# Kernel optimization log

Measured on AMD Instinct MI355X. Metric: run time of the kernel, lower is better.

## Reference

```python
import jax, jax.numpy as jnp
import numpy as np

N_NODES = 50000
N_EDGES = 800000
D_IN, H, D_OUT = 128, 128, 64


def setup_inputs() -> dict:
    key = jax.random.key(0)
    ks = jax.random.split(key, 8)
    x = jax.random.normal(ks[0], (N_NODES, D_IN), dtype=jnp.float32)
    edge_index = jax.random.randint(ks[1], (2, N_EDGES), 0, N_NODES, dtype=jnp.int64)
    s = 0.05
    return {
        "x": x,
        "edge_index": edge_index,
        # PyG Linear weights are [out, in]; y = x @ W.T + b
        "W_rel1": jax.random.normal(ks[2], (H, D_IN), dtype=jnp.float32) * s,
        "W_root1": jax.random.normal(ks[3], (H, D_IN), dtype=jnp.float32) * s,
        "b1": jax.random.normal(ks[4], (H,), dtype=jnp.float32) * s,
        "W_rel2": jax.random.normal(ks[5], (D_OUT, H), dtype=jnp.float32) * s,
        "W_root2": jax.random.normal(ks[6], (D_OUT, H), dtype=jnp.float32) * s,
        "b2": jax.random.normal(ks[7], (D_OUT,), dtype=jnp.float32) * s,
    }


def graph_conv(x, src, dst, W_rel, W_root, b):
    # sum-aggregate raw neighbor features, then apply linear (equivalent to
    # transforming each message first, but cheaper: one gather + one GEMM).
    agg = jax.ops.segment_sum(x[src], dst, num_segments=N_NODES)  # [N, D]
    return jnp.einsum('nd,hd->nh', agg, W_rel) \
         + jnp.einsum('nd,hd->nh', x, W_root) + b


def reference(x, edge_index, W_rel1, W_root1, b1, W_rel2, W_root2, b2):
    src, dst = edge_index[0], edge_index[1]  # messages flow src -> dst
    t = jax.nn.relu(graph_conv(x, src, dst, W_rel1, W_root1, b1))
    t = graph_conv(t, src, dst, W_rel2, W_root2, b2)
    return t
```

## Files before the change

### kernel.cpp

```cpp
#include <hip/hip_runtime.h>

#define NNODES 50000
#define DIM 128
#define SCAN_CHUNK 4096
#define NSCAN 13
#define PREP_BLOCKS 3200
#define POISON ((int)0xAAAAAAAA)

typedef __attribute__((ext_vector_type(8))) __bf16 bf16x8;
typedef __attribute__((ext_vector_type(4))) float f32x4;

__device__ inline unsigned short f2b(float f) {
    unsigned int u = __float_as_uint(f);
    u += 0x7fffu + ((u >> 16) & 1u);
    return (unsigned short)(u >> 16);
}
__device__ inline float blo(unsigned int u) { return __uint_as_float(u << 16); }
__device__ inline float bhi(unsigned int u) { return __uint_as_float(u & 0xffff0000u); }
__device__ inline unsigned int pack2(float a, float b) {
    return (unsigned int)f2b(a) | ((unsigned int)f2b(b) << 16);
}

__global__ __launch_bounds__(256) void k_prep(
    const float* __restrict__ x, unsigned short* __restrict__ xb, int n4,
    const float* __restrict__ Wa1, const float* __restrict__ Wb1,
    const float* __restrict__ Wa2, const float* __restrict__ Wb2,
    unsigned short* __restrict__ wa1, unsigned short* __restrict__ wb1,
    unsigned short* __restrict__ wa2, unsigned short* __restrict__ wb2,
    const int* __restrict__ dst, int* __restrict__ counts,
    unsigned short* __restrict__ rank, int n_edges)
{
    const int gid = blockIdx.x * 256 + threadIdx.x;

    const int i1 = blockIdx.x * 512 + threadIdx.x;
    const int i2 = i1 + 256;
    const bool ok1 = i1 < n4, ok2 = i2 < n4;
    float4 v1, v2;
    if (ok1) v1 = reinterpret_cast<const float4*>(x)[i1];
    if (ok2) v2 = reinterpret_cast<const float4*>(x)[i2];

    if (gid < n_edges) {
        const int rep = threadIdx.x & 3;
        int rk = atomicAdd(&counts[rep * NNODES + dst[gid]], 1) - POISON;
        rank[gid] = (unsigned short)(rk | (rep << 14));
    }

    if (gid < 16384) { wa1[gid] = f2b(Wa1[gid]); wb1[gid] = f2b(Wb1[gid]); }
    if (gid < 8192)  { wa2[gid] = f2b(Wa2[gid]); wb2[gid] = f2b(Wb2[gid]); }

    if (ok1) {
        uint2 o;
        o.x = pack2(v1.x, v1.y);
        o.y = pack2(v1.z, v1.w);
        reinterpret_cast<uint2*>(xb)[i1] = o;
    }
    if (ok2) {
        uint2 o;
        o.x = pack2(v2.x, v2.y);
        o.y = pack2(v2.z, v2.w);
        reinterpret_cast<uint2*>(xb)[i2] = o;
    }
}

__global__ __launch_bounds__(1024) void k_scan_local(
    const int* __restrict__ counts, int* __restrict__ rowptr,
    int* __restrict__ bsum, uint2* __restrict__ repx2, int n)
{
    __shared__ int wsum[16];
    const int lane = threadIdx.x & 63;
    const int wid = threadIdx.x >> 6;
    int i = blockIdx.x * SCAN_CHUNK + threadIdx.x * 4;
    int4 v = make_int4(0, 0, 0, 0);
    if (i + 3 < n) {
        int4 c0 = *reinterpret_cast<const int4*>(counts + i);
        int4 c1 = *reinterpret_cast<const int4*>(counts + NNODES + i);
        int4 c2 = *reinterpret_cast<const int4*>(counts + 2 * NNODES + i);
        int4 c3 = *reinterpret_cast<const int4*>(counts + 3 * NNODES + i);
        c0.x -= POISON; c0.y -= POISON; c0.z -= POISON; c0.w -= POISON;
        c1.x -= POISON; c1.y -= POISON; c1.z -= POISON; c1.w -= POISON;
        c2.x -= POISON; c2.y -= POISON; c2.z -= POISON; c2.w -= POISON;
        c3.x -= POISON; c3.y -= POISON; c3.z -= POISON; c3.w -= POISON;
        v.x = c0.x + c1.x + c2.x + c3.x;
        v.y = c0.y + c1.y + c2.y + c3.y;
        v.z = c0.z + c1.z + c2.z + c3.z;
        v.w = c0.w + c1.w + c2.w + c3.w;
        uint2 r0, r1g, r2g, r3g;
        r0.x  = (unsigned)(c0.x) << 16;
        r0.y  = (unsigned)(c0.x + c1.x) | ((unsigned)(c0.x + c1.x + c2.x) << 16);
        r1g.x = (unsigned)(c0.y) << 16;
        r1g.y = (unsigned)(c0.y + c1.y) | ((unsigned)(c0.y + c1.y + c2.y) << 16);
        r2g.x = (unsigned)(c0.z) << 16;
        r2g.y = (unsigned)(c0.z + c1.z) | ((unsigned)(c0.z + c1.z + c2.z) << 16);
        r3g.x = (unsigned)(c0.w) << 16;
        r3g.y = (unsigned)(c0.w + c1.w) | ((unsigned)(c0.w + c1.w + c2.w) << 16);
        repx2[i + 0] = r0;
        repx2[i + 1] = r1g;
        repx2[i + 2] = r2g;
        repx2[i + 3] = r3g;
    } else {
#pragma unroll
        for (int j = 0; j < 3; ++j) {
            if (i + j < n) {
                int c0 = counts[i + j] - POISON;
                int c1 = counts[NNODES + i + j] - POISON;
                int c2 = counts[2 * NNODES + i + j] - POISON;
                int c3 = counts[3 * NNODES + i + j] - POISON;
                int t = c0 + c1 + c2 + c3;
                if (j == 0) v.x = t; else if (j == 1) v.y = t; else v.z = t;
                uint2 r;
                r.x = (unsigned)c0 << 16;
                r.y = (unsigned)(c0 + c1) | ((unsigned)(c0 + c1 + c2) << 16);
                repx2[i + j] = r;
            }
        }
    }
    int tot = v.x + v.y + v.z + v.w;
    int s = tot;
#pragma unroll
    for (int off = 1; off < 64; off <<= 1) {
        int t = __shfl_up(s, off);
        if (lane >= off) s += t;
    }
    if (lane == 63) wsum[wid] = s;
    __syncthreads();
    if (wid == 0 && lane < 16) {
        int ws = wsum[lane];
#pragma unroll
        for (int off = 1; off < 16; off <<= 1) {
            int t = __shfl_up(ws, off);
            if (lane >= off) ws += t;
        }
        wsum[lane] = ws;
    }
    __syncthreads();
    int prefix = ((wid > 0) ? wsum[wid - 1] : 0) + (s - tot);
    int4 o;
    o.x = prefix;
    o.y = prefix + v.x;
    o.z = o.y + v.y;
    o.w = o.z + v.z;
    if (i + 3 <= n) {
        *reinterpret_cast<int4*>(rowptr + i) = o;
    } else {
        if (i + 0 <= n) rowptr[i + 0] = o.x;
        if (i + 1 <= n) rowptr[i + 1] = o.y;
        if (i + 2 <= n) rowptr[i + 2] = o.z;
    }
    if (threadIdx.x == 1023) bsum[blockIdx.x] = wsum[15];
}

__device__ inline void build_prefix_lds(const int* __restrict__ bsum, int* pre) {
    if (threadIdx.x < 16) {
        int off = 0;
#pragma unroll 1
        for (int j = 0; j < NSCAN && j < (int)threadIdx.x; ++j) off += bsum[j];
        pre[threadIdx.x] = off;
    }
    __syncthreads();
}

__device__ inline int rep_off(uint2 rp, int r) {
    unsigned pw = (r & 2) ? rp.y : rp.x;
    return (r & 1) ? (int)(pw >> 16) : (int)(pw & 0xffffu);
}

__global__ __launch_bounds__(256) void k_place(
    const int* __restrict__ src, const int* __restrict__ dst,
    const unsigned short* __restrict__ rank, const int* __restrict__ rowptr,
    const int* __restrict__ bsum, const uint2* __restrict__ repx2,
    unsigned short* __restrict__ srcs_sorted, int n_edges)
{
    __shared__ int pre[16];
    build_prefix_lds(bsum, pre);
    int e = (blockIdx.x * 256 + threadIdx.x) * 8;
    if (e + 7 < n_edges) {
        int4 s4a = *reinterpret_cast<const int4*>(src + e);
        int4 s4b = *reinterpret_cast<const int4*>(src + e + 4);
        int4 d4a = *reinterpret_cast<const int4*>(dst + e);
        int4 d4b = *reinterpret_cast<const int4*>(dst + e + 4);
        uint4 r8 = *reinterpret_cast<const uint4*>(rank + e);
        unsigned rk[8];
        rk[0] = r8.x & 0xffffu; rk[1] = r8.x >> 16;
        rk[2] = r8.y & 0xffffu; rk[3] = r8.y >> 16;
        rk[4] = r8.z & 0xffffu; rk[5] = r8.z >> 16;
        rk[6] = r8.w & 0xffffu; rk[7] = r8.w >> 16;
        int dd[8] = {d4a.x, d4a.y, d4a.z, d4a.w, d4b.x, d4b.y, d4b.z, d4b.w};
        int ss[8] = {s4a.x, s4a.y, s4a.z, s4a.w, s4b.x, s4b.y, s4b.z, s4b.w};
#pragma unroll
        for (int j = 0; j < 8; ++j) {
            const int d = dd[j];
            const int r = (int)(rk[j] >> 14);
            const int rv = (int)(rk[j] & 0x3fffu);
            uint2 rp = repx2[d];
            srcs_sorted[rowptr[d] + pre[d >> 12] + rep_off(rp, r) + rv] =
                (unsigned short)ss[j];
        }
    } else {
        for (; e < n_edges; ++e) {
            int d = dst[e];
            unsigned rk16 = rank[e];
            int r = (int)(rk16 >> 14);
            int rv = (int)(rk16 & 0x3fffu);
            uint2 rp = repx2[d];
            srcs_sorted[rowptr[d] + pre[d >> 12] + rep_off(rp, r) + rv] =
                (unsigned short)src[e];
        }
    }
}

__global__ __launch_bounds__(256) void k_fused1(
    const unsigned short* __restrict__ xb,
    const int* __restrict__ rowptr, const int* __restrict__ bsum,
    const unsigned short* __restrict__ srcs,
    const unsigned short* __restrict__ Wr1,
    const unsigned short* __restrict__ Wo1,
    const float* __restrict__ b1,
    const unsigned short* __restrict__ Wr2,
    const unsigned short* __restrict__ Wo2,
    const float* __restrict__ b2,
    unsigned short* __restrict__ U2,
    unsigned short* __restrict__ R2)
{
    __shared__ int pre[16];
    __shared__ __align__(16) unsigned short agg[16][136];
    __shared__ __align__(16) unsigned short xt[16][136];
    __shared__ __align__(16) unsigned short tt[16][136];
    build_prefix_lds(bsum, pre);

    const int tid = threadIdx.x;
    const int nl = tid >> 4;
    const int node = blockIdx.x * 16 + nl;
    const int seg = tid & 15;

    {
        *reinterpret_cast<uint4*>(&xt[nl][seg * 8]) =
            *reinterpret_cast<const uint4*>(xb + (size_t)node * DIM + seg * 8);

        int beg = rowptr[node] + pre[node >> 12];
        int end = rowptr[node + 1] + pre[(node + 1) >> 12];
        float acc[8];
#pragma unroll
        for (int i = 0; i < 8; ++i) acc[i] = 0.f;
        int e = beg;
#pragma unroll 1
        for (; e + 7 < end; e += 8) {
            uint4 v[8];
#pragma unroll
            for (int u = 0; u < 8; ++u) {
                int s = srcs[e + u];
                v[u] = *reinterpret_cast<const uint4*>(xb + (size_t)s * DIM + seg * 8);
            }
#pragma unroll
            for (int u = 0; u < 8; ++u) {
                acc[0] += blo(v[u].x); acc[1] += bhi(v[u].x);
                acc[2] += blo(v[u].y); acc[3] += bhi(v[u].y);
                acc[4] += blo(v[u].z); acc[5] += bhi(v[u].z);
                acc[6] += blo(v[u].w); acc[7] += bhi(v[u].w);
            }
        }
#pragma unroll 1
        for (; e + 1 < end; e += 2) {
            int s0 = srcs[e], s1 = srcs[e + 1];
            uint4 v0 = *reinterpret_cast<const uint4*>(xb + (size_t)s0 * DIM + seg * 8);
            uint4 v1 = *reinterpret_cast<const uint4*>(xb + (size_t)s1 * DIM + seg * 8);
            acc[0] += blo(v0.x) + blo(v1.x); acc[1] += bhi(v0.x) + bhi(v1.x);
            acc[2] += blo(v0.y) + blo(v1.y); acc[3] += bhi(v0.y) + bhi(v1.y);
            acc[4] += blo(v0.z) + blo(v1.z); acc[5] += bhi(v0.z) + bhi(v1.z);
            acc[6] += blo(v0.w) + blo(v1.w); acc[7] += bhi(v0.w) + bhi(v1.w);
        }
        if (e < end) {
            int s0 = srcs[e];
            uint4 v = *reinterpret_cast<const uint4*>(xb + (size_t)s0 * DIM + seg * 8);
            acc[0] += blo(v.x); acc[1] += bhi(v.x);
            acc[2] += blo(v.y); acc[3] += bhi(v.y);
            acc[4] += blo(v.z); acc[5] += bhi(v.z);
            acc[6] += blo(v.w); acc[7] += bhi(v.w);
        }
        uint4 o;
        o.x = pack2(acc[0], acc[1]);
        o.y = pack2(acc[2], acc[3]);
        o.z = pack2(acc[4], acc[5]);
        o.w = pack2(acc[6], acc[7]);
        *reinterpret_cast<uint4*>(&agg[nl][seg * 8]) = o;
    }
    __syncthreads();

    const int wave = tid >> 6;
    const int lane = tid & 63;
    const int quad = lane >> 4;
    const int l16 = lane & 15;

    {
        f32x4 at0 = {0.f, 0.f, 0.f, 0.f};
        f32x4 at1 = {0.f, 0.f, 0.f, 0.f};
#pragma unroll
        for (int kk = 0; kk < 4; ++kk) {
            const int ko = kk * 32;
            bf16x8 af = *reinterpret_cast<const bf16x8*>(&agg[l16][ko + quad * 8]);
            bf16x8 xf = *reinterpret_cast<const bf16x8*>(&xt[l16][ko + quad * 8]);
            const size_t w0 = (size_t)(wave * 32 + l16) * DIM + ko + quad * 8;
            const size_t w1 = w0 + (size_t)16 * DIM;
            bf16x8 wr0 = *reinterpret_cast<const bf16x8*>(Wr1 + w0);
            bf16x8 wo0 = *reinterpret_cast<const bf16x8*>(Wo1 + w0);
            bf16x8 wr1 = *reinterpret_cast<const bf16x8*>(Wr1 + w1);
            bf16x8 wo1 = *reinterpret_cast<const bf16x8*>(Wo1 + w1);
            at0 = __builtin_amdgcn_mfma_f32_16x16x32_bf16(wr0, af, at0, 0, 0, 0);
            at0 = __builtin_amdgcn_mfma_f32_16x16x32_bf16(wo0, xf, at0, 0, 0, 0);
            at1 = __builtin_amdgcn_mfma_f32_16x16x32_bf16(wr1, af, at1, 0, 0, 0);
            at1 = __builtin_amdgcn_mfma_f32_16x16x32_bf16(wo1, xf, at1, 0, 0, 0);
        }
        {
            const int colb0 = wave * 32 + quad * 4;
            const float4 bv0 = *reinterpret_cast<const float4*>(b1 + colb0);
            uint2 t0;
            t0.x = pack2(fmaxf(at0[0] + bv0.x, 0.f), fmaxf(at0[1] + bv0.y, 0.f));
            t0.y = pack2(fmaxf(at0[2] + bv0.z, 0.f), fmaxf(at0[3] + bv0.w, 0.f));
            *reinterpret_cast<uint2*>(&tt[l16][colb0]) = t0;
            const int colb1 = colb0 + 16;
            const float4 bv1 = *reinterpret_cast<const float4*>(b1 + colb1);
            uint2 t1;
            t1.x = pack2(fmaxf(at1[0] + bv1.x, 0.f), fmaxf(at1[1] + bv1.y, 0.f));
            t1.y = pack2(fmaxf(at1[2] + bv1.z, 0.f), fmaxf(at1[3] + bv1.w, 0.f));
            *reinterpret_cast<uint2*>(&tt[l16][colb1]) = t1;
        }
    }
    __syncthreads();

    f32x4 aU = {0.f, 0.f, 0.f, 0.f};
    f32x4 aR = {0.f, 0.f, 0.f, 0.f};
#pragma unroll
    for (int kk = 0; kk < 4; ++kk) {
        const int ko = kk * 32;
        bf16x8 xf = *reinterpret_cast<const bf16x8*>(&tt[l16][ko + quad * 8]);
        const size_t woff = (size_t)(wave * 16 + l16) * DIM + ko + quad * 8;
        bf16x8 wu = *reinterpret_cast<const bf16x8*>(Wr2 + woff);
        bf16x8 wrg = *reinterpret_cast<const bf16x8*>(Wo2 + woff);
        aU = __builtin_amdgcn_mfma_f32_16x16x32_bf16(wu, xf, aU, 0, 0, 0);
        aR = __builtin_amdgcn_mfma_f32_16x16x32_bf16(wrg, xf, aR, 0, 0, 0);
    }
    const int onode = blockIdx.x * 16 + l16;
    const int colb = wave * 16 + quad * 4;
    const float4 bv = *reinterpret_cast<const float4*>(b2 + colb);
    uint2 uo, ro;
    uo.x = pack2(aU[0], aU[1]);
    uo.y = pack2(aU[2], aU[3]);
    ro.x = pack2(aR[0] + bv.x, aR[1] + bv.y);
    ro.y = pack2(aR[2] + bv.z, aR[3] + bv.w);
    *reinterpret_cast<uint2*>(U2 + (size_t)onode * 64 + colb) = uo;
    *reinterpret_cast<uint2*>(R2 + (size_t)onode * 64 + colb) = ro;
}

__global__ __launch_bounds__(256) void k_gather_ep2(
    const unsigned short* __restrict__ U, const unsigned short* __restrict__ R,
    const int* __restrict__ rowptr, const int* __restrict__ bsum,
    const unsigned short* __restrict__ srcs, float* __restrict__ out)
{
    __shared__ int pre[16];
    build_prefix_lds(bsum, pre);
    int node = blockIdx.x * 32 + (threadIdx.x >> 3);
    if (node >= NNODES) return;
    int seg = threadIdx.x & 7;
    int beg = rowptr[node] + pre[node >> 12];
    int end = rowptr[node + 1] + pre[(node + 1) >> 12];
    float acc[8];
#pragma unroll
    for (int i = 0; i < 8; ++i) acc[i] = 0.f;
    int e = beg;
#pragma unroll 1
    for (; e + 7 < end; e += 8) {
        uint4 v[8];
#pragma unroll
        for (int u = 0; u < 8; ++u) {
            int s = srcs[e + u];
            v[u] = *reinterpret_cast<const uint4*>(U + (size_t)s * 64 + seg * 8);
        }
#pragma unroll
        for (int u = 0; u < 8; ++u) {
            acc[0] += blo(v[u].x); acc[1] += bhi(v[u].x);
            acc[2] += blo(v[u].y); acc[3] += bhi(v[u].y);
            acc[4] += blo(v[u].z); acc[5] += bhi(v[u].z);
            acc[6] += blo(v[u].w); acc[7] += bhi(v[u].w);
        }
    }
#pragma unroll 1
    for (; e + 1 < end; e += 2) {
        int s0 = srcs[e], s1 = srcs[e + 1];
        uint4 v0 = *reinterpret_cast<const uint4*>(U + (size_t)s0 * 64 + seg * 8);
        uint4 v1 = *reinterpret_cast<const uint4*>(U + (size_t)s1 * 64 + seg * 8);
        acc[0] += blo(v0.x) + blo(v1.x); acc[1] += bhi(v0.x) + bhi(v1.x);
        acc[2] += blo(v0.y) + blo(v1.y); acc[3] += bhi(v0.y) + bhi(v1.y);
        acc[4] += blo(v0.z) + blo(v1.z); acc[5] += bhi(v0.z) + bhi(v1.z);
        acc[6] += blo(v0.w) + blo(v1.w); acc[7] += bhi(v0.w) + bhi(v1.w);
    }
    if (e < end) {
        int s0 = srcs[e];
        uint4 v = *reinterpret_cast<const uint4*>(U + (size_t)s0 * 64 + seg * 8);
        acc[0] += blo(v.x); acc[1] += bhi(v.x);
        acc[2] += blo(v.y); acc[3] += bhi(v.y);
        acc[4] += blo(v.z); acc[5] += bhi(v.z);
        acc[6] += blo(v.w); acc[7] += bhi(v.w);
    }
    uint4 rv = *reinterpret_cast<const uint4*>(R + (size_t)node * 64 + seg * 8);
    acc[0] += blo(rv.x); acc[1] += bhi(rv.x);
    acc[2] += blo(rv.y); acc[3] += bhi(rv.y);
    acc[4] += blo(rv.z); acc[5] += bhi(rv.z);
    acc[6] += blo(rv.w); acc[7] += bhi(rv.w);
    float4 o0 = make_float4(acc[0], acc[1], acc[2], acc[3]);
    float4 o1 = make_float4(acc[4], acc[5], acc[6], acc[7]);
    float* op = out + (size_t)node * 64 + seg * 8;
    *reinterpret_cast<float4*>(op) = o0;
    *reinterpret_cast<float4*>(op + 4) = o1;
}

extern "C" void kernel_launch(void* const* d_in, const int* in_sizes, int n_in,
                              void* d_out, int out_size, void* d_ws, size_t ws_size,
                              hipStream_t stream) {
    const float* x       = (const float*)d_in[0];
    const int*   ei      = (const int*)d_in[1];
    const float* W_rel1  = (const float*)d_in[2];
    const float* W_root1 = (const float*)d_in[3];
    const float* b1      = (const float*)d_in[4];
    const float* W_rel2  = (const float*)d_in[5];
    const float* W_root2 = (const float*)d_in[6];
    const float* b2      = (const float*)d_in[7];

    const int n_edges = in_sizes[1] / 2;
    const int* src = ei;
    const int* dst = ei + n_edges;

    const size_t NELEM = (size_t)NNODES * DIM;
    unsigned short* xb   = (unsigned short*)d_ws;
    unsigned short* u2   = xb + NELEM;
    unsigned short* r2   = u2 + (size_t)NNODES * 64;
    unsigned short* wa1  = r2 + (size_t)NNODES * 64;
    unsigned short* wb1  = wa1 + 16384;
    unsigned short* wa2  = wb1 + 16384;
    unsigned short* wb2  = wa2 + 8192;
    int* counts = (int*)(wb2 + 8192);
    int* rowptr = counts + 4 * NNODES;
    int* bsum   = rowptr + (NNODES + 4);
    uint2* repx2 = (uint2*)(bsum + 20);
    unsigned short* rank16 = (unsigned short*)(repx2 + NNODES);
    unsigned short* srcs16 = rank16 + n_edges;

    float* out = (float*)d_out;

    const int n4 = NNODES * DIM / 4;
    const int pblocks = (n_edges + 2047) / 2048;
    const int f1blocks = NNODES / 16;
    const int g2blocks = (NNODES + 31) / 32;
    const int sblocks = NSCAN;

    k_prep<<<PREP_BLOCKS, 256, 0, stream>>>(
        x, xb, n4, W_rel1, W_root1, W_rel2, W_root2,
        wa1, wb1, wa2, wb2, dst, counts, rank16, n_edges);

    k_scan_local<<<sblocks, 1024, 0, stream>>>(counts, rowptr, bsum, repx2, NNODES);

    k_place<<<pblocks, 256, 0, stream>>>(src, dst, rank16, rowptr, bsum, repx2,
                                         srcs16, n_edges);

    k_fused1<<<f1blocks, 256, 0, stream>>>(
        xb, rowptr, bsum, srcs16, wa1, wb1, b1, wa2, wb2, b2, u2, r2);

    k_gather_ep2<<<g2blocks, 256, 0, stream>>>(u2, r2, rowptr, bsum, srcs16, out);
}
```

Measured before the change: 216.2 us.

## Shrink fused layer-1 kernel to one wave per 16-node block

Rewrites k_fused1 to run one 64-thread wave per block instead of four waves. The wave loops over four passes to gather the 16 nodes' neighbor sums, then loops over all output column tiles for both GEMMs, holding the A fragments in registers. The xt LDS tile is removed and x-row fragments are read directly from global memory. The aim is to raise occupancy through smaller blocks with less LDS and cheaper barriers. The cost is that each wave does four times the serial gather and MFMA work, with less latency hiding inside a block.

```diff
diff --git a/kernel.cpp b/kernel.cpp
--- a/kernel.cpp
+++ b/kernel.cpp
@@ -208,7 +208,7 @@
     }
 }
 
-__global__ __launch_bounds__(256) void k_fused1(
+__global__ __launch_bounds__(64) void k_fused1(
     const unsigned short* __restrict__ xb,
     const int* __restrict__ rowptr, const int* __restrict__ bsum,
     const unsigned short* __restrict__ srcs,
@@ -223,19 +223,18 @@
 {
     __shared__ int pre[16];
     __shared__ __align__(16) unsigned short agg[16][136];
-    __shared__ __align__(16) unsigned short xt[16][136];
     __shared__ __align__(16) unsigned short tt[16][136];
     build_prefix_lds(bsum, pre);
 
-    const int tid = threadIdx.x;
-    const int nl = tid >> 4;
-    const int node = blockIdx.x * 16 + nl;
-    const int seg = tid & 15;
-
-    {
-        *reinterpret_cast<uint4*>(&xt[nl][seg * 8]) =
-            *reinterpret_cast<const uint4*>(xb + (size_t)node * DIM + seg * 8);
-
+    const int lane = threadIdx.x;
+    const int grp = lane >> 4;
+    const int seg = lane & 15;
+    const int base = blockIdx.x * 16;
+
+#pragma unroll 1
+    for (int p = 0; p < 4; ++p) {
+        const int nl = p * 4 + grp;
+        const int node = base + nl;
         int beg = rowptr[node] + pre[node >> 12];
         int end = rowptr[node + 1] + pre[(node + 1) >> 12];
         float acc[8];
@@ -285,69 +284,65 @@
     }
     __syncthreads();
 
-    const int wave = tid >> 6;
-    const int lane = tid & 63;
     const int quad = lane >> 4;
     const int l16 = lane & 15;
-
-    {
-        f32x4 at0 = {0.f, 0.f, 0.f, 0.f};
-        f32x4 at1 = {0.f, 0.f, 0.f, 0.f};
+    const int node = base + l16;
+
+    bf16x8 af[4], xf[4];
+#pragma unroll
+    for (int kk = 0; kk < 4; ++kk) {
+        af[kk] = *reinterpret_cast<const bf16x8*>(&agg[l16][kk * 32 + quad * 8]);
+        xf[kk] = *reinterpret_cast<const bf16x8*>(
+            xb + (size_t)node * DIM + kk * 32 + quad * 8);
+    }
+
+#pragma unroll 1
+    for (int s = 0; s < 8; ++s) {
+        f32x4 a = {0.f, 0.f, 0.f, 0.f};
 #pragma unroll
         for (int kk = 0; kk < 4; ++kk) {
-            const int ko = kk * 32;
-            bf16x8 af = *reinterpret_cast<const bf16x8*>(&agg[l16][ko + quad * 8]);
-            bf16x8 xf = *reinterpret_cast<const bf16x8*>(&xt[l16][ko + quad * 8]);
-            const size_t w0 = (size_t)(wave * 32 + l16) * DIM + ko + quad * 8;
-            const size_t w1 = w0 + (size_t)16 * DIM;
-            bf16x8 wr0 = *reinterpret_cast<const bf16x8*>(Wr1 + w0);
-            bf16x8 wo0 = *reinterpret_cast<const bf16x8*>(Wo1 + w0);
-            bf16x8 wr1 = *reinterpret_cast<const bf16x8*>(Wr1 + w1);
-            bf16x8 wo1 = *reinterpret_cast<const bf16x8*>(Wo1 + w1);
-            at0 = __builtin_amdgcn_mfma_f32_16x16x32_bf16(wr0, af, at0, 0, 0, 0);
-            at0 = __builtin_amdgcn_mfma_f32_16x16x32_bf16(wo0, xf, at0, 0, 0, 0);
-            at1 = __builtin_amdgcn_mfma_f32_16x16x32_bf16(wr1, af, at1, 0, 0, 0);
-            at1 = __builtin_amdgcn_mfma_f32_16x16x32_bf16(wo1, xf, at1, 0, 0, 0);
-        }
-        {
-            const int colb0 = wave * 32 + quad * 4;
-            const float4 bv0 = *reinterpret_cast<const float4*>(b1 + colb0);
-            uint2 t0;
-            t0.x = pack2(fmaxf(at0[0] + bv0.x, 0.f), fmaxf(at0[1] + bv0.y, 0.f));
-            t0.y = pack2(fmaxf(at0[2] + bv0.z, 0.f), fmaxf(at0[3] + bv0.w, 0.f));
-            *reinterpret_cast<uint2*>(&tt[l16][colb0]) = t0;
-            const int colb1 = colb0 + 16;
-            const float4 bv1 = *reinterpret_cast<const float4*>(b1 + colb1);
-            uint2 t1;
-            t1.x = pack2(fmaxf(at1[0] + bv1.x, 0.f), fmaxf(at1[1] + bv1.y, 0.f));
-            t1.y = pack2(fmaxf(at1[2] + bv1.z, 0.f), fmaxf(at1[3] + bv1.w, 0.f));
-            *reinterpret_cast<uint2*>(&tt[l16][colb1]) = t1;
-        }
+            const size_t w = (size_t)(s * 16 + l16) * DIM + kk * 32 + quad * 8;
+            bf16x8 wr = *reinterpret_cast<const bf16x8*>(Wr1 + w);
+            bf16x8 wo = *reinterpret_cast<const bf16x8*>(Wo1 + w);
+            a = __builtin_amdgcn_mfma_f32_16x16x32_bf16(wr, af[kk], a, 0, 0, 0);
+            a = __builtin_amdgcn_mfma_f32_16x16x32_bf16(wo, xf[kk], a, 0, 0, 0);
+        }
+        const int colb = s * 16 + quad * 4;
+        const float4 bv = *reinterpret_cast<const float4*>(b1 + colb);
+        uint2 t;
+        t.x = pack2(fmaxf(a[0] + bv.x, 0.f), fmaxf(a[1] + bv.y, 0.f));
+        t.y = pack2(fmaxf(a[2] + bv.z, 0.f), fmaxf(a[3] + bv.w, 0.f));
+        *reinterpret_cast<uint2*>(&tt[l16][colb]) = t;
     }
     __syncthreads();
 
-    f32x4 aU = {0.f, 0.f, 0.f, 0.f};
-    f32x4 aR = {0.f, 0.f, 0.f, 0.f};
-#pragma unroll
-    for (int kk = 0; kk < 4; ++kk) {
-        const int ko = kk * 32;
-        bf16x8 xf = *reinterpret_cast<const bf16x8*>(&tt[l16][ko + quad * 8]);
-        const size_t woff = (size_t)(wave * 16 + l16) * DIM + ko + quad * 8;
-        bf16x8 wu = *reinterpret_cast<const bf16x8*>(Wr2 + woff);
-        bf16x8 wrg = *reinterpret_cast<const bf16x8*>(Wo2 + woff);
-        aU = __builtin_amdgcn_mfma_f32_16x16x32_bf16(wu, xf, aU, 0, 0, 0);
-        aR = __builtin_amdgcn_mfma_f32_16x16x32_bf16(wrg, xf, aR, 0, 0, 0);
-    }
-    const int onode = blockIdx.x * 16 + l16;
-    const int colb = wave * 16 + quad * 4;
-    const float4 bv = *reinterpret_cast<const float4*>(b2 + colb);
-    uint2 uo, ro;
-    uo.x = pack2(aU[0], aU[1]);
-    uo.y = pack2(aU[2], aU[3]);
-    ro.x = pack2(aR[0] + bv.x, aR[1] + bv.y);
-    ro.y = pack2(aR[2] + bv.z, aR[3] + bv.w);
-    *reinterpret_cast<uint2*>(U2 + (size_t)onode * 64 + colb) = uo;
-    *reinterpret_cast<uint2*>(R2 + (size_t)onode * 64 + colb) = ro;
+    bf16x8 tf[4];
+#pragma unroll
+    for (int kk = 0; kk < 4; ++kk)
+        tf[kk] = *reinterpret_cast<const bf16x8*>(&tt[l16][kk * 32 + quad * 8]);
+
+#pragma unroll 1
+    for (int s = 0; s < 4; ++s) {
+        f32x4 aU = {0.f, 0.f, 0.f, 0.f};
+        f32x4 aR = {0.f, 0.f, 0.f, 0.f};
+#pragma unroll
+        for (int kk = 0; kk < 4; ++kk) {
+            const size_t w = (size_t)(s * 16 + l16) * DIM + kk * 32 + quad * 8;
+            bf16x8 wu = *reinterpret_cast<const bf16x8*>(Wr2 + w);
+            bf16x8 wo = *reinterpret_cast<const bf16x8*>(Wo2 + w);
+            aU = __builtin_amdgcn_mfma_f32_16x16x32_bf16(wu, tf[kk], aU, 0, 0, 0);
+            aR = __builtin_amdgcn_mfma_f32_16x16x32_bf16(wo, tf[kk], aR, 0, 0, 0);
+        }
+        const int colb = s * 16 + quad * 4;
+        const float4 bv = *reinterpret_cast<const float4*>(b2 + colb);
+        uint2 uo, ro;
+        uo.x = pack2(aU[0], aU[1]);
+        uo.y = pack2(aU[2], aU[3]);
+        ro.x = pack2(aR[0] + bv.x, aR[1] + bv.y);
+        ro.y = pack2(aR[2] + bv.z, aR[3] + bv.w);
+        *reinterpret_cast<uint2*>(U2 + (size_t)node * 64 + colb) = uo;
+        *reinterpret_cast<uint2*>(R2 + (size_t)node * 64 + colb) = ro;
+    }
 }
 
 __global__ __launch_bounds__(256) void k_gather_ep2(
@@ -460,7 +455,7 @@
     k_place<<<pblocks, 256, 0, stream>>>(src, dst, rank16, rowptr, bsum, repx2,
                                          srcs16, n_edges);
 
-    k_fused1<<<f1blocks, 256, 0, stream>>>(
+    k_fused1<<<f1blocks, 64, 0, stream>>>(
         xb, rowptr, bsum, srcs16, wa1, wb1, b1, wa2, wb2, b2, u2, r2);
 
     k_gather_ep2<<<g2blocks, 256, 0, stream>>>(u2, r2, rowptr, bsum, srcs16, out);
```

Result: no change. 218.1 us (+0.9%).

## Sort nodes by in-degree so fused layer-1 blocks process similar-degree nodes

Applied to the files above, without the earlier changes.

Adds a per-chunk degree histogram and rank in the scan kernel, a prefix scan over degree bins inside an extra block of the placement kernel, and a new kernel that builds a node permutation ordered by degree. The fused layer-1 kernel then processes the nodes of each 16-node block through this permutation, so the threads sharing a block handle similar-degree nodes and load imbalance within a block shrinks. The cost is an extra kernel launch, more workspace, and scattered reads and writes of xb, U2 and R2 through the permutation.

```diff
diff --git a/kernel.cpp b/kernel.cpp
--- a/kernel.cpp
+++ b/kernel.cpp
@@ -64,9 +64,12 @@
 
 __global__ __launch_bounds__(1024) void k_scan_local(
     const int* __restrict__ counts, int* __restrict__ rowptr,
-    int* __restrict__ bsum, uint2* __restrict__ repx2, int n)
+    int* __restrict__ bsum, uint2* __restrict__ repx2,
+    int* __restrict__ dbin2, unsigned short* __restrict__ drank, int n)
 {
     __shared__ int wsum[16];
+    __shared__ int dh[256];
+    if (threadIdx.x < 256) dh[threadIdx.x] = 0;
     const int lane = threadIdx.x & 63;
     const int wid = threadIdx.x >> 6;
     int i = blockIdx.x * SCAN_CHUNK + threadIdx.x * 4;
@@ -114,6 +117,26 @@
             }
         }
     }
+    __syncthreads();
+    if (i + 3 < n) {
+        int d0 = v.x < 255 ? v.x : 255;
+        int d1 = v.y < 255 ? v.y : 255;
+        int d2 = v.z < 255 ? v.z : 255;
+        int d3 = v.w < 255 ? v.w : 255;
+        drank[i + 0] = (unsigned short)atomicAdd(&dh[d0], 1);
+        drank[i + 1] = (unsigned short)atomicAdd(&dh[d1], 1);
+        drank[i + 2] = (unsigned short)atomicAdd(&dh[d2], 1);
+        drank[i + 3] = (unsigned short)atomicAdd(&dh[d3], 1);
+    } else {
+#pragma unroll
+        for (int j = 0; j < 3; ++j) {
+            if (i + j < n) {
+                int dv = (j == 0) ? v.x : (j == 1) ? v.y : v.z;
+                if (dv > 255) dv = 255;
+                drank[i + j] = (unsigned short)atomicAdd(&dh[dv], 1);
+            }
+        }
+    }
     int tot = v.x + v.y + v.z + v.w;
     int s = tot;
 #pragma unroll
@@ -147,6 +170,7 @@
         if (i + 2 <= n) rowptr[i + 2] = o.z;
     }
     if (threadIdx.x == 1023) bsum[blockIdx.x] = wsum[15];
+    if (threadIdx.x < 256) dbin2[blockIdx.x * 256 + threadIdx.x] = dh[threadIdx.x];
 }
 
 __device__ inline void build_prefix_lds(const int* __restrict__ bsum, int* pre) {
@@ -168,11 +192,34 @@
     const int* __restrict__ src, const int* __restrict__ dst,
     const unsigned short* __restrict__ rank, const int* __restrict__ rowptr,
     const int* __restrict__ bsum, const uint2* __restrict__ repx2,
-    unsigned short* __restrict__ srcs_sorted, int n_edges)
+    unsigned short* __restrict__ srcs_sorted, int n_edges,
+    const int* __restrict__ dbin2, int* __restrict__ offt)
 {
+    if (blockIdx.x == 0) {
+        __shared__ int ps[256];
+        const int d = threadIdx.x;
+        int c[NSCAN];
+        int t = 0;
+#pragma unroll
+        for (int b = 0; b < NSCAN; ++b) { c[b] = dbin2[b * 256 + d]; t += c[b]; }
+        ps[d] = t;
+        __syncthreads();
+#pragma unroll
+        for (int o = 1; o < 256; o <<= 1) {
+            int val = (d >= o) ? ps[d - o] : 0;
+            __syncthreads();
+            ps[d] += val;
+            __syncthreads();
+        }
+        int run = ps[d] - t;
+#pragma unroll
+        for (int b = 0; b < NSCAN; ++b) { offt[b * 256 + d] = run; run += c[b]; }
+        return;
+    }
+
     __shared__ int pre[16];
     build_prefix_lds(bsum, pre);
-    int e = (blockIdx.x * 256 + threadIdx.x) * 8;
+    int e = ((int)(blockIdx.x - 1) * 256 + threadIdx.x) * 8;
     if (e + 7 < n_edges) {
         int4 s4a = *reinterpret_cast<const int4*>(src + e);
         int4 s4b = *reinterpret_cast<const int4*>(src + e + 4);
@@ -208,10 +255,28 @@
     }
 }
 
-__global__ __launch_bounds__(256) void k_fused1(
+__global__ __launch_bounds__(256) void k_permplace(
+    const int* __restrict__ rowptr, const int* __restrict__ bsum,
+    const int* __restrict__ offt, const unsigned short* __restrict__ drank,
+    unsigned short* __restrict__ perm)
+{
+    __shared__ int pre[16];
+    build_prefix_lds(bsum, pre);
+    int n = blockIdx.x * 256 + threadIdx.x;
+    if (n >= NNODES) return;
+    int g0 = rowptr[n] + pre[n >> 12];
+    int g1 = rowptr[n + 1] + pre[(n + 1) >> 12];
+    int d = g1 - g0;
+    if (d > 255) d = 255;
+    int slot = offt[(n >> 12) * 256 + d] + (int)drank[n];
+    perm[slot] = (unsigned short)n;
+}
+
+__global__ __launch_bounds__(256) void k_fusedA(
     const unsigned short* __restrict__ xb,
     const int* __restrict__ rowptr, const int* __restrict__ bsum,
     const unsigned short* __restrict__ srcs,
+    const unsigned short* __restrict__ perm,
     const unsigned short* __restrict__ Wr1,
     const unsigned short* __restrict__ Wo1,
     const float* __restrict__ b1,
@@ -222,6 +287,8 @@
     unsigned short* __restrict__ R2)
 {
     __shared__ int pre[16];
+    __shared__ int pnd[16];
+    __shared__ int nbeg[16], nend[16];
     __shared__ __align__(16) unsigned short agg[16][136];
     __shared__ __align__(16) unsigned short xt[16][136];
     __shared__ __align__(16) unsigned short tt[16][136];
@@ -229,15 +296,24 @@
 
     const int tid = threadIdx.x;
     const int nl = tid >> 4;
-    const int node = blockIdx.x * 16 + nl;
     const int seg = tid & 15;
+    const int base = blockIdx.x * 16;
+
+    if (tid < 16) {
+        int pn = perm[base + tid];
+        pnd[tid] = pn;
+        nbeg[tid] = rowptr[pn] + pre[pn >> 12];
+        nend[tid] = rowptr[pn + 1] + pre[(pn + 1) >> 12];
+    }
+    __syncthreads();
 
     {
+        const int node = pnd[nl];
         *reinterpret_cast<uint4*>(&xt[nl][seg * 8]) =
             *reinterpret_cast<const uint4*>(xb + (size_t)node * DIM + seg * 8);
 
-        int beg = rowptr[node] + pre[node >> 12];
-        int end = rowptr[node + 1] + pre[(node + 1) >> 12];
+        int beg = nbeg[nl];
+        int end = nend[nl];
         float acc[8];
 #pragma unroll
         for (int i = 0; i < 8; ++i) acc[i] = 0.f;
@@ -289,6 +365,7 @@
     const int lane = tid & 63;
     const int quad = lane >> 4;
     const int l16 = lane & 15;
+    const int onode = pnd[l16];
 
     {
         f32x4 at0 = {0.f, 0.f, 0.f, 0.f};
@@ -338,7 +415,6 @@
         aU = __builtin_amdgcn_mfma_f32_16x16x32_bf16(wu, xf, aU, 0, 0, 0);
         aR = __builtin_amdgcn_mfma_f32_16x16x32_bf16(wrg, xf, aR, 0, 0, 0);
     }
-    const int onode = blockIdx.x * 16 + l16;
     const int colb = wave * 16 + quad * 4;
     const float4 bv = *reinterpret_cast<const float4*>(b2 + colb);
     uint2 uo, ro;
@@ -442,26 +518,34 @@
     uint2* repx2 = (uint2*)(bsum + 20);
     unsigned short* rank16 = (unsigned short*)(repx2 + NNODES);
     unsigned short* srcs16 = rank16 + n_edges;
+    int* dbin2 = (int*)(srcs16 + n_edges);
+    int* offt  = dbin2 + NSCAN * 256;
+    unsigned short* drank = (unsigned short*)(offt + NSCAN * 256);
+    unsigned short* perm  = drank + NNODES;
 
     float* out = (float*)d_out;
 
     const int n4 = NNODES * DIM / 4;
     const int pblocks = (n_edges + 2047) / 2048;
-    const int f1blocks = NNODES / 16;
+    const int fablocks = NNODES / 16;
     const int g2blocks = (NNODES + 31) / 32;
+    const int ppblocks = (NNODES + 255) / 256;
     const int sblocks = NSCAN;
 
     k_prep<<<PREP_BLOCKS, 256, 0, stream>>>(
         x, xb, n4, W_rel1, W_root1, W_rel2, W_root2,
         wa1, wb1, wa2, wb2, dst, counts, rank16, n_edges);
 
-    k_scan_local<<<sblocks, 1024, 0, stream>>>(counts, rowptr, bsum, repx2, NNODES);
-
-    k_place<<<pblocks, 256, 0, stream>>>(src, dst, rank16, rowptr, bsum, repx2,
-                                         srcs16, n_edges);
-
-    k_fused1<<<f1blocks, 256, 0, stream>>>(
-        xb, rowptr, bsum, srcs16, wa1, wb1, b1, wa2, wb2, b2, u2, r2);
+    k_scan_local<<<sblocks, 1024, 0, stream>>>(counts, rowptr, bsum, repx2,
+                                               dbin2, drank, NNODES);
+
+    k_place<<<pblocks + 1, 256, 0, stream>>>(src, dst, rank16, rowptr, bsum,
+                                             repx2, srcs16, n_edges, dbin2, offt);
+
+    k_permplace<<<ppblocks, 256, 0, stream>>>(rowptr, bsum, offt, drank, perm);
+
+    k_fusedA<<<fablocks, 256, 0, stream>>>(
+        xb, rowptr, bsum, srcs16, perm, wa1, wb1, b1, wa2, wb2, b2, u2, r2);
 
     k_gather_ep2<<<g2blocks, 256, 0, stream>>>(u2, r2, rowptr, bsum, srcs16, out);
 }
```

Result: no change. 212.9 us (-1.5%).
